# Kernel optimization log

Hardware: AMD Instinct MI355X
Metric: run time of the kernel (lower is better)

## Reference

```python
import jax, jax.numpy as jnp
import numpy as np

NUM_QUBITS = 12
ENC_COPIES = 1
ANSATZ_COPIES = 2
BATCH = 1024
NUM_THETAS = NUM_QUBITS * (ANSATZ_COPIES + 1) * 2  # 72

_H = jnp.asarray(np.array([[1.0, 1.0], [1.0, -1.0]], np.complex64) / np.sqrt(2.0))


def _apply_1q(state, U, q):
    # state: [B, 2, 2, ..., 2] (n qubit axes); apply 2x2 unitary U on qubit q
    s = jnp.moveaxis(state, 1 + q, -1)
    s = jnp.einsum('...j,ij->...i', s, U)
    return jnp.moveaxis(s, -1, 1 + q)


def _apply_zpow(state, t, q):
    # cirq Z**t = diag(1, e^{i*pi*t}); t is scalar or per-batch [B]
    n = state.ndim - 1
    phase = jnp.exp(1j * jnp.pi * t).astype(jnp.complex64)
    factor = jnp.stack([jnp.ones_like(phase), phase], axis=-1)
    if factor.ndim == 2:  # batched exponent -> broadcast over other qubit axes
        factor = factor.reshape((factor.shape[0],) + (1,) * (n - 1) + (2,))
    s = jnp.moveaxis(state, 1 + q, -1)
    return jnp.moveaxis(s * factor, -1, 1 + q)


def _ypow_unitary(t):
    # cirq Y**t up to global phase e^{i*pi*t/2} (irrelevant for Z expectations)
    a = 0.5 * jnp.pi * t
    c, s = jnp.cos(a), jnp.sin(a)
    return jnp.stack([jnp.stack([c, -s]), jnp.stack([s, c])]).astype(jnp.complex64)


def _apply_cnot(state, c, t):
    s = jnp.moveaxis(state, (1 + c, 1 + t), (-2, -1))
    s = jnp.stack([s[..., 0, :], s[..., 1, ::-1]], axis=-2)
    return jnp.moveaxis(s, (-2, -1), (1 + c, 1 + t))


def _encoding_block(state, x):
    # FirstOrderPauliZEncoding: per copy, per qubit: H then Z**x_q
    for _ in range(ENC_COPIES):
        for q in range(NUM_QUBITS):
            state = _apply_1q(state, _H, q)
            state = _apply_zpow(state, x[:, q], q)
    return state


def _ansatz_block(state, th, with_cnot):
    # EfficientSU2 layer: Y**th[q,0], Z**th[q,1] per qubit, then CNOT chain
    for q in range(NUM_QUBITS):
        state = _apply_1q(state, _ypow_unitary(th[q, 0]), q)
        state = _apply_zpow(state, th[q, 1], q)
    if with_cnot:
        for q in range(NUM_QUBITS - 1):
            state = _apply_cnot(state, q, q + 1)
    return state


_enc = jax.checkpoint(_encoding_block)
_ans_cnot = jax.checkpoint(lambda st, th: _ansatz_block(st, th, True))
_ans_last = jax.checkpoint(lambda st, th: _ansatz_block(st, th, False))


def _circuit(inputs, thetas):
    b = inputs.shape[0]
    state = jnp.zeros((b, 2 ** NUM_QUBITS), jnp.complex64).at[:, 0].set(1.0)
    state = state.reshape((b,) + (2,) * NUM_QUBITS)
    state = _enc(state, inputs)
    th = thetas.reshape(ANSATZ_COPIES + 1, NUM_QUBITS, 2)
    for l in range(ANSATZ_COPIES + 1):
        state = (_ans_cnot if l < ANSATZ_COPIES else _ans_last)(state, th[l])
    # readouts: <Z_q> for each qubit
    probs = state.real ** 2 + state.imag ** 2
    exps = []
    for q in range(NUM_QUBITS):
        axes = tuple(a for a in range(1, NUM_QUBITS + 1) if a != 1 + q)
        p = probs.sum(axis=axes)  # [B, 2]
        exps.append(p[:, 0] - p[:, 1])
    return jnp.stack(exps, axis=-1)  # [B, NUM_QUBITS]


def setup_inputs() -> dict:
    key = jax.random.key(0)
    k1, k2 = jax.random.split(key)
    inputs = jax.random.uniform(k1, (BATCH, NUM_QUBITS), jnp.float32)
    thetas = jax.random.uniform(k2, (NUM_THETAS,), jnp.float32, minval=-1.0, maxval=1.0)
    return {"inputs": inputs, "thetas": thetas}


def reference(inputs, thetas):
    return _circuit(inputs, thetas)
```

## Files before the change

### kernel.cpp

```cpp
#include <hip/hip_runtime.h>


#define PI_F 3.14159265358979323846f
#define NR 16

__device__ __forceinline__ float2 cmul(float2 a, float2 b) {
    return make_float2(a.x*b.x - a.y*b.y, a.x*b.y + a.y*b.x);
}
__device__ __forceinline__ float2 cmulc(float2 a, float2 b) {
    return make_float2(a.x*b.x + a.y*b.y, a.y*b.x - a.x*b.y);
}

template<int RB>
__device__ __forceinline__ void ypow_reg(float2 (&a)[NR], float c, float s) {
    #pragma unroll
    for (int r0 = 0; r0 < NR; ++r0) {
        if ((r0 >> RB) & 1) continue;
        const int r1 = r0 | (1 << RB);
        float2 a0 = a[r0], a1 = a[r1];
        a[r0] = make_float2(c*a0.x - s*a1.x, c*a0.y - s*a1.y);
        a[r1] = make_float2(s*a0.x + c*a1.x, s*a0.y + c*a1.y);
    }
}

__device__ __forceinline__ void ypowA(float2 (&a)[NR], const float* __restrict__ th) {
    { float s,c; __sincosf(0.5f*PI_F*th[4],  &s,&c); ypow_reg<3>(a,c,s); }
    { float s,c; __sincosf(0.5f*PI_F*th[6],  &s,&c); ypow_reg<2>(a,c,s); }
    { float s,c; __sincosf(0.5f*PI_F*th[8],  &s,&c); ypow_reg<1>(a,c,s); }
    { float s,c; __sincosf(0.5f*PI_F*th[10], &s,&c); ypow_reg<0>(a,c,s); }
}
__device__ __forceinline__ void ypowB(float2 (&a)[NR], const float* __restrict__ th) {
    { float s,c; __sincosf(0.5f*PI_F*th[16], &s,&c); ypow_reg<3>(a,c,s); }
    { float s,c; __sincosf(0.5f*PI_F*th[18], &s,&c); ypow_reg<2>(a,c,s); }
    { float s,c; __sincosf(0.5f*PI_F*th[20], &s,&c); ypow_reg<1>(a,c,s); }
    { float s,c; __sincosf(0.5f*PI_F*th[22], &s,&c); ypow_reg<0>(a,c,s); }
}

template<bool PRE_SYNC>
__device__ __forceinline__ void exchange_AB(float2 (&a)[NR], char* bufc,
                                            int w, int lane,
                                            float c6, float s6, float c7, float s7) {
    if (PRE_SYNC) __syncthreads();
    const int wbyte = (w << 13) | ((lane & 15) << 5) | ((lane >> 4) << 3);
    #pragma unroll
    for (int r = 0; r < NR; ++r)
        *(float2*)(bufc + ((wbyte | (r << 9)) ^ ((r & 7) << 4))) = a[r];
    asm volatile("s_waitcnt lgkmcnt(0)" ::: "memory");
    const int g = lane >> 2;
    const float y60 = (lane & 2) ? s6 : c6;
    const float y61 = (lane & 2) ? c6 : -s6;
    const float y70 = (lane & 1) ? s7 : c7;
    const float y71 = (lane & 1) ? c7 : -s7;
    const float k00 = y60*y70, k01 = y60*y71, k10 = y61*y70, k11 = y61*y71;
    const int rbyte = (w << 13) | (g << 9);
    const int kx = (g & 7) << 4;
    #pragma unroll
    for (int R = 0; R < NR; ++R) {
        const int base = rbyte | (R << 5);
        float4 p01 = *(const float4*)(bufc + (base ^ kx));
        float4 p23 = *(const float4*)(bufc + ((base | 16) ^ kx));
        a[R] = make_float2(k00*p01.x + k01*p01.z + k10*p23.x + k11*p23.z,
                           k00*p01.y + k01*p01.w + k10*p23.y + k11*p23.w);
        if ((R & 3) == 3) asm volatile("" ::: "memory");
    }
}

__device__ __forceinline__ void exchange_BA(float2 (&a)[NR], char* bufc,
                                            int w, int lane,
                                            float c0, float s0, float c1, float s1) {
    __syncthreads();
    const int v_  = (w >> 1) & 1;
    const int u_  = v_ ^ (w & 1);
    const int l5u = (lane >> 5) ^ u_;
    const int wbyte = (l5u << 14) | ((lane & 31) << 9) | (u_ << 4) | (v_ << 3);
    const int wkx = (lane & 7) << 4;
    #pragma unroll
    for (int R = 0; R < NR; ++R)
        *(float2*)(bufc + ((wbyte | (R << 5)) ^ wkx)) = a[R];
    __syncthreads();
    const float ky00 = (w & 2) ? s0 : c0;
    const float ky01 = (w & 2) ? c0 : -s0;
    const float ky10 = (w & 1) ? s1 : c1;
    const float ky11 = (w & 1) ? c1 : -s1;
    const float k00 = ky10*ky00, k01 = ky10*ky01, k10 = ky11*ky00, k11 = ky11*ky01;
    #pragma unroll
    for (int r = 0; r < NR; ++r) {
        const int ylow = (r << 6) | lane;
        const int t = ylow ^ (ylow >> 1);
        const int base = t << 5;
        const int kx = t & 0x70;
        float4 p01 = *(const float4*)(bufc + (base ^ kx));
        float4 p23 = *(const float4*)(bufc + ((base | 16) ^ kx));
        a[r] = make_float2(k00*p01.x + k01*p01.z + k10*p23.x + k11*p23.z,
                           k00*p01.y + k01*p01.w + k10*p23.y + k11*p23.w);
        if ((r & 3) == 3) asm volatile("" ::: "memory");
    }
}

__device__ __forceinline__ void fused_z_B(float2 (&a)[NR], int w, int lane,
                                          const float* __restrict__ th) {
    float alpha = ((w & 2) ? th[1] : 0.0f) + ((w & 1) ? th[3] : 0.0f);
    #pragma unroll
    for (int k = 0; k < 6; ++k)
        alpha += ((lane >> k) & 1) ? th[2*(7-k)+1] : 0.0f;
    float2 zb; __sincosf(PI_F * alpha, &zb.y, &zb.x);
    float2 zq[4];
    #pragma unroll
    for (int j = 0; j < 4; ++j)
        __sincosf(PI_F * th[2*(11-j)+1], &zq[j].y, &zq[j].x);
    float2 cur = zb;
    a[0] = cmul(a[0], cur);
    #pragma unroll
    for (int k = 1; k < NR; ++k) {
        const int bit = __builtin_ctz(k);
        const int g = k ^ (k >> 1);
        cur = ((g >> bit) & 1) ? cmul(cur, zq[bit]) : cmulc(cur, zq[bit]);
        a[g] = cmul(a[g], cur);
    }
}

__global__ __launch_bounds__(256) void vqc_kernel(
    const float* __restrict__ inputs,
    const float* __restrict__ thetas,
    float* __restrict__ out)
{
    __shared__ __align__(16) char bufc[32768];
    __shared__ float redBuf[48];

    const int b = blockIdx.x;
    const int tid = threadIdx.x;
    const int w = tid >> 6;
    const int lane = tid & 63;
    const float* x = inputs + b * 12;

    float2 a[NR];

    float phb = 0.0f;
    #pragma unroll
    for (int k = 0; k < 6; ++k)
        phb += ((lane >> k) & 1) ? x[11 - k] : 0.0f;
    float2 cisb; __sincosf(PI_F * phb, &cisb.y, &cisb.x);
    float2 E0; __sincosf(PI_F * x[0], &E0.y, &E0.x);
    float2 E1; __sincosf(PI_F * x[1], &E1.y, &E1.x);
    float sa, ca; __sincosf(0.5f * PI_F * thetas[0], &sa, &ca);
    float sb, cb; __sincosf(0.5f * PI_F * thetas[2], &sb, &cb);
    float2 F0 = (w & 2) ? make_float2(sa + ca*E0.x,  ca*E0.y)
                        : make_float2(ca - sa*E0.x, -sa*E0.y);
    float2 F1 = (w & 1) ? make_float2(sb + cb*E1.x,  cb*E1.y)
                        : make_float2(cb - sb*E1.x, -sb*E1.y);
    float2 g0 = cmul(cmul(F0, F1), cisb);
    g0.x *= 0.015625f; g0.y *= 0.015625f;
    float2 zr[4];
    #pragma unroll
    for (int j = 0; j < 4; ++j)
        __sincosf(PI_F * x[5 - j], &zr[j].y, &zr[j].x);
    {
        float2 cur = g0;
        a[0] = cur;
        #pragma unroll
        for (int k = 1; k < NR; ++k) {
            const int bit = __builtin_ctz(k);
            const int g = k ^ (k >> 1);
            cur = ((g >> bit) & 1) ? cmul(cur, zr[bit]) : cmulc(cur, zr[bit]);
            a[g] = cur;
        }
    }

    const float* th0 = thetas;
    const float* th1 = thetas + 24;
    const float* th2 = thetas + 48;

    ypowA(a, th0);
    { float s6,c6,s7,c7;
      __sincosf(0.5f*PI_F*th0[12], &s6,&c6);
      __sincosf(0.5f*PI_F*th0[14], &s7,&c7);
      exchange_AB<false>(a, bufc, w, lane, c6,s6,c7,s7); }
    ypowB(a, th0);
    fused_z_B(a, w, lane, th0);
    { float s0,c0,s1,c1;
      __sincosf(0.5f*PI_F*th1[0], &s0,&c0);
      __sincosf(0.5f*PI_F*th1[2], &s1,&c1);
      exchange_BA(a, bufc, w, lane, c0,s0,c1,s1); }

    ypowA(a, th1);
    { float s6,c6,s7,c7;
      __sincosf(0.5f*PI_F*th1[12], &s6,&c6);
      __sincosf(0.5f*PI_F*th1[14], &s7,&c7);
      exchange_AB<true>(a, bufc, w, lane, c6,s6,c7,s7); }
    ypowB(a, th1);
    fused_z_B(a, w, lane, th1);
    { float s0,c0,s1,c1;
      __sincosf(0.5f*PI_F*th2[0], &s0,&c0);
      __sincosf(0.5f*PI_F*th2[2], &s1,&c1);
      exchange_BA(a, bufc, w, lane, c0,s0,c1,s1); }

    ypowA(a, th2);
    { float s6,c6,s7,c7;
      __sincosf(0.5f*PI_F*th2[12], &s6,&c6);
      __sincosf(0.5f*PI_F*th2[14], &s7,&c7);
      exchange_AB<true>(a, bufc, w, lane, c6,s6,c7,s7); }
    ypowB(a, th2);

    float totalP = 0.0f;
    float D[4] = {0, 0, 0, 0};
    #pragma unroll
    for (int r = 0; r < NR; ++r) {
        const float p = a[r].x * a[r].x + a[r].y * a[r].y;
        totalP += p;
        #pragma unroll
        for (int j = 0; j < 4; ++j)
            D[j] += ((r >> j) & 1) ? -p : p;
    }
    #pragma unroll
    for (int q = 0; q < 12; ++q) {
        float v;
        if (q == 0)      v = (w & 2) ? -totalP : totalP;
        else if (q == 1) v = (w & 1) ? -totalP : totalP;
        else if (q <= 7) v = ((lane >> (7 - q)) & 1) ? -totalP : totalP;
        else             v = D[11 - q];
        #pragma unroll
        for (int off = 32; off >= 1; off >>= 1)
            v += __shfl_xor(v, off, 64);
        if (lane == 0) redBuf[w * 12 + q] = v;
    }
    __syncthreads();
    if (tid < 12)
        out[b * 12 + tid] = redBuf[tid] + redBuf[12 + tid]
                          + redBuf[24 + tid] + redBuf[36 + tid];
}

extern "C" void kernel_launch(void* const* d_in, const int* in_sizes, int n_in,
                              void* d_out, int out_size, void* d_ws, size_t ws_size,
                              hipStream_t stream) {
    const float* inputs = (const float*)d_in[0];
    const float* thetas = (const float*)d_in[1];
    float* out = (float*)d_out;
    vqc_kernel<<<dim3(1024), dim3(256), 0, stream>>>(inputs, thetas, out);
}
```

Measured before the change: 84.67 us.

## Apply mid-qubit Y rotations via lane shuffles and drop AB LDS exchange

Changes the state layout so that six of the qubits live on lane bits, and applies their Y rotations with cross-lane shuffles instead of register pairs. This removes the AB shared-memory transpose, leaving one LDS exchange per layer instead of two. It also reuses the shared buffer for the final reduction. In exchange it adds 12 shuffles per register per layer, uses a new XOR swizzle for the remaining exchange, and inserts an extra barrier before the reduction.

```diff
diff --git a/kernel.cpp b/kernel.cpp
--- a/kernel.cpp
+++ b/kernel.cpp
@@ -23,12 +23,18 @@
     }
 }
 
-__device__ __forceinline__ void ypowA(float2 (&a)[NR], const float* __restrict__ th) {
-    { float s,c; __sincosf(0.5f*PI_F*th[4],  &s,&c); ypow_reg<3>(a,c,s); }
-    { float s,c; __sincosf(0.5f*PI_F*th[6],  &s,&c); ypow_reg<2>(a,c,s); }
-    { float s,c; __sincosf(0.5f*PI_F*th[8],  &s,&c); ypow_reg<1>(a,c,s); }
-    { float s,c; __sincosf(0.5f*PI_F*th[10], &s,&c); ypow_reg<0>(a,c,s); }
-}
+template<int M>
+__device__ __forceinline__ void ypow_lane(float2 (&a)[NR], int lane, float c, float s) {
+    const float k1 = (lane & M) ? s : -s;
+    #pragma unroll
+    for (int r = 0; r < NR; ++r) {
+        float px = __shfl_xor(a[r].x, M, 64);
+        float py = __shfl_xor(a[r].y, M, 64);
+        a[r].x = c*a[r].x + k1*px;
+        a[r].y = c*a[r].y + k1*py;
+    }
+}
+
 __device__ __forceinline__ void ypowB(float2 (&a)[NR], const float* __restrict__ th) {
     { float s,c; __sincosf(0.5f*PI_F*th[16], &s,&c); ypow_reg<3>(a,c,s); }
     { float s,c; __sincosf(0.5f*PI_F*th[18], &s,&c); ypow_reg<2>(a,c,s); }
@@ -36,47 +42,30 @@
     { float s,c; __sincosf(0.5f*PI_F*th[22], &s,&c); ypow_reg<0>(a,c,s); }
 }
 
-template<bool PRE_SYNC>
-__device__ __forceinline__ void exchange_AB(float2 (&a)[NR], char* bufc,
-                                            int w, int lane,
-                                            float c6, float s6, float c7, float s7) {
-    if (PRE_SYNC) __syncthreads();
-    const int wbyte = (w << 13) | ((lane & 15) << 5) | ((lane >> 4) << 3);
-    #pragma unroll
-    for (int r = 0; r < NR; ++r)
-        *(float2*)(bufc + ((wbyte | (r << 9)) ^ ((r & 7) << 4))) = a[r];
-    asm volatile("s_waitcnt lgkmcnt(0)" ::: "memory");
-    const int g = lane >> 2;
-    const float y60 = (lane & 2) ? s6 : c6;
-    const float y61 = (lane & 2) ? c6 : -s6;
-    const float y70 = (lane & 1) ? s7 : c7;
-    const float y71 = (lane & 1) ? c7 : -s7;
-    const float k00 = y60*y70, k01 = y60*y71, k10 = y61*y70, k11 = y61*y71;
-    const int rbyte = (w << 13) | (g << 9);
-    const int kx = (g & 7) << 4;
-    #pragma unroll
-    for (int R = 0; R < NR; ++R) {
-        const int base = rbyte | (R << 5);
-        float4 p01 = *(const float4*)(bufc + (base ^ kx));
-        float4 p23 = *(const float4*)(bufc + ((base | 16) ^ kx));
-        a[R] = make_float2(k00*p01.x + k01*p01.z + k10*p23.x + k11*p23.z,
-                           k00*p01.y + k01*p01.w + k10*p23.y + k11*p23.w);
-        if ((R & 3) == 3) asm volatile("" ::: "memory");
-    }
-}
-
-__device__ __forceinline__ void exchange_BA(float2 (&a)[NR], char* bufc,
-                                            int w, int lane,
+__device__ __forceinline__ void ypow_lanes(float2 (&a)[NR], int lane,
+                                           const float* __restrict__ th) {
+    { float s,c; __sincosf(0.5f*PI_F*th[4],  &s,&c); ypow_lane<32>(a,lane,c,s); }
+    { float s,c; __sincosf(0.5f*PI_F*th[6],  &s,&c); ypow_lane<16>(a,lane,c,s); }
+    { float s,c; __sincosf(0.5f*PI_F*th[8],  &s,&c); ypow_lane<8>(a,lane,c,s); }
+    { float s,c; __sincosf(0.5f*PI_F*th[10], &s,&c); ypow_lane<4>(a,lane,c,s); }
+    { float s,c; __sincosf(0.5f*PI_F*th[12], &s,&c); ypow_lane<2>(a,lane,c,s); }
+    { float s,c; __sincosf(0.5f*PI_F*th[14], &s,&c); ypow_lane<1>(a,lane,c,s); }
+}
+
+__device__ __forceinline__ void exchange_BB(float2 (&a)[NR], char* bufc,
+                                            int w, int lane, bool preSync,
                                             float c0, float s0, float c1, float s1) {
-    __syncthreads();
-    const int v_  = (w >> 1) & 1;
-    const int u_  = v_ ^ (w & 1);
-    const int l5u = (lane >> 5) ^ u_;
-    const int wbyte = (l5u << 14) | ((lane & 31) << 9) | (u_ << 4) | (v_ << 3);
-    const int wkx = (lane & 7) << 4;
-    #pragma unroll
-    for (int R = 0; R < NR; ++R)
-        *(float2*)(bufc + ((wbyte | (R << 5)) ^ wkx)) = a[R];
+    if (preSync) __syncthreads();
+    const int v_ = (w >> 1) & 1;
+    const int u_ = v_ ^ (w & 1);
+    const int s9 = ((lane >> 5) ^ u_) & 1;
+    const int wbyte = (s9 << 14) | ((lane & 31) << 9) | (u_ << 4) | (v_ << 3);
+    #pragma unroll
+    for (int r = 0; r < NR; ++r) {
+        const int byt = wbyte | (r << 5);
+        const int key = (((byt >> 9) ^ (byt >> 12)) & 7) << 4;
+        *(float2*)(bufc + (byt ^ key)) = a[r];
+    }
     __syncthreads();
     const float ky00 = (w & 2) ? s0 : c0;
     const float ky01 = (w & 2) ? c0 : -s0;
@@ -85,12 +74,12 @@
     const float k00 = ky10*ky00, k01 = ky10*ky01, k10 = ky11*ky00, k11 = ky11*ky01;
     #pragma unroll
     for (int r = 0; r < NR; ++r) {
-        const int ylow = (r << 6) | lane;
+        const int ylow = (lane << 4) | r;
         const int t = ylow ^ (ylow >> 1);
         const int base = t << 5;
-        const int kx = t & 0x70;
-        float4 p01 = *(const float4*)(bufc + (base ^ kx));
-        float4 p23 = *(const float4*)(bufc + ((base | 16) ^ kx));
+        const int key = (((base >> 9) ^ (base >> 12)) & 7) << 4;
+        float4 p01 = *(const float4*)(bufc + (base ^ key));
+        float4 p23 = *(const float4*)(bufc + ((base | 16) ^ key));
         a[r] = make_float2(k00*p01.x + k01*p01.z + k10*p23.x + k11*p23.z,
                            k00*p01.y + k01*p01.w + k10*p23.y + k11*p23.w);
         if ((r & 3) == 3) asm volatile("" ::: "memory");
@@ -125,7 +114,6 @@
     float* __restrict__ out)
 {
     __shared__ __align__(16) char bufc[32768];
-    __shared__ float redBuf[48];
 
     const int b = blockIdx.x;
     const int tid = threadIdx.x;
@@ -138,7 +126,7 @@
     float phb = 0.0f;
     #pragma unroll
     for (int k = 0; k < 6; ++k)
-        phb += ((lane >> k) & 1) ? x[11 - k] : 0.0f;
+        phb += ((lane >> k) & 1) ? x[7 - k] : 0.0f;
     float2 cisb; __sincosf(PI_F * phb, &cisb.y, &cisb.x);
     float2 E0; __sincosf(PI_F * x[0], &E0.y, &E0.x);
     float2 E1; __sincosf(PI_F * x[1], &E1.y, &E1.x);
@@ -153,7 +141,7 @@
     float2 zr[4];
     #pragma unroll
     for (int j = 0; j < 4; ++j)
-        __sincosf(PI_F * x[5 - j], &zr[j].y, &zr[j].x);
+        __sincosf(PI_F * x[11 - j], &zr[j].y, &zr[j].x);
     {
         float2 cur = g0;
         a[0] = cur;
@@ -170,36 +158,24 @@
     const float* th1 = thetas + 24;
     const float* th2 = thetas + 48;
 
-    ypowA(a, th0);
-    { float s6,c6,s7,c7;
-      __sincosf(0.5f*PI_F*th0[12], &s6,&c6);
-      __sincosf(0.5f*PI_F*th0[14], &s7,&c7);
-      exchange_AB<false>(a, bufc, w, lane, c6,s6,c7,s7); }
     ypowB(a, th0);
+    ypow_lanes(a, lane, th0);
     fused_z_B(a, w, lane, th0);
     { float s0,c0,s1,c1;
       __sincosf(0.5f*PI_F*th1[0], &s0,&c0);
       __sincosf(0.5f*PI_F*th1[2], &s1,&c1);
-      exchange_BA(a, bufc, w, lane, c0,s0,c1,s1); }
-
-    ypowA(a, th1);
-    { float s6,c6,s7,c7;
-      __sincosf(0.5f*PI_F*th1[12], &s6,&c6);
-      __sincosf(0.5f*PI_F*th1[14], &s7,&c7);
-      exchange_AB<true>(a, bufc, w, lane, c6,s6,c7,s7); }
+      exchange_BB(a, bufc, w, lane, false, c0,s0,c1,s1); }
+
     ypowB(a, th1);
+    ypow_lanes(a, lane, th1);
     fused_z_B(a, w, lane, th1);
     { float s0,c0,s1,c1;
       __sincosf(0.5f*PI_F*th2[0], &s0,&c0);
       __sincosf(0.5f*PI_F*th2[2], &s1,&c1);
-      exchange_BA(a, bufc, w, lane, c0,s0,c1,s1); }
-
-    ypowA(a, th2);
-    { float s6,c6,s7,c7;
-      __sincosf(0.5f*PI_F*th2[12], &s6,&c6);
-      __sincosf(0.5f*PI_F*th2[14], &s7,&c7);
-      exchange_AB<true>(a, bufc, w, lane, c6,s6,c7,s7); }
+      exchange_BB(a, bufc, w, lane, true, c0,s0,c1,s1); }
+
     ypowB(a, th2);
+    ypow_lanes(a, lane, th2);
 
     float totalP = 0.0f;
     float D[4] = {0, 0, 0, 0};
@@ -211,6 +187,8 @@
         for (int j = 0; j < 4; ++j)
             D[j] += ((r >> j) & 1) ? -p : p;
     }
+    float* redBuf = (float*)bufc;
+    __syncthreads();
     #pragma unroll
     for (int q = 0; q < 12; ++q) {
         float v;
```

Result: slower. 95.00 us (+12.2%).
